# Kernel tuning notes

Measured on AMD Instinct MI355X. Metric: run time of the kernel, lower is better.

## Reference

```python
import jax, jax.numpy as jnp
import numpy as np

D = 1024
H = 16
B = 4
S = 2048
NEG = -1000000000.0


def setup_inputs() -> dict:
    key = jax.random.key(0)
    ks = jax.random.split(key, 12)
    s = 0.02
    inp = {
        "Q": jax.random.normal(ks[0], (B, S, D), jnp.float32),
        "K": jax.random.normal(ks[1], (B, S, D), jnp.float32),
        "V": jax.random.normal(ks[2], (B, S, D), jnp.float32),
        # causal mask, broadcastable to [B, H, S, S]
        "mask": jnp.broadcast_to(jnp.tril(jnp.ones((S, S), bool)), (B, 1, S, S)),
        "Wq": jax.random.normal(ks[3], (D, D), jnp.float32) * s,
        "bq": jnp.zeros((D,), jnp.float32),
        "Wk": jax.random.normal(ks[4], (D, D), jnp.float32) * s,
        "bk": jnp.zeros((D,), jnp.float32),
        "Wv": jax.random.normal(ks[5], (D, D), jnp.float32) * s,
        "bv": jnp.zeros((D,), jnp.float32),
        "Wo": jax.random.normal(ks[6], (D, D), jnp.float32) * s,
        "bo": jnp.zeros((D,), jnp.float32),
    }
    return inp


def reference(Q, K, V, mask, Wq, bq, Wk, bk, Wv, bv, Wo, bo):
    d = D // H  # head dim
    def split(x):  # [B,S,D] -> [B,H,S,d]
        Bx, Sx, _ = x.shape
        return x.reshape(Bx, Sx, H, d).transpose(0, 2, 1, 3)

    q = split(Q @ Wq + bq)
    k = split(K @ Wk + bk)
    v = split(V @ Wv + bv)

    scores = jnp.einsum("bhsd,bhtd->bhst", q, k) / jnp.sqrt(jnp.float32(d))
    scores = jnp.where(mask, scores, NEG)
    attn = jax.nn.softmax(scores, axis=-1)
    out = jnp.einsum("bhst,bhtd->bhsd", attn, v)  # [B,H,S,d]
    out = out.transpose(0, 2, 1, 3).reshape(Q.shape[0], Q.shape[1], D)
    return out @ Wo + bo
```

## Files before the change

### kernel.cpp

```cpp
#include <hip/hip_runtime.h>
#include <hip/hip_bf16.h>
#include <type_traits>

#define DEV __device__ __forceinline__

typedef short bf16x8 __attribute__((ext_vector_type(8)));
typedef float f32x4 __attribute__((ext_vector_type(4)));
typedef float f32x16 __attribute__((ext_vector_type(16)));
typedef unsigned u32x4 __attribute__((ext_vector_type(4)));

static DEV unsigned short f2bf(float f) {
  unsigned u = __builtin_bit_cast(unsigned, f);
  u += 0x7FFFu + ((u >> 16) & 1u);
  return (unsigned short)(u >> 16);
}

static DEV unsigned cvtpk(float lo, float hi) {
  unsigned d;
  asm("v_cvt_pk_bf16_f32 %0, %1, %2" : "=v"(d) : "v"(lo), "v"(hi));
  return d;
}

static DEV void pl32(unsigned& x, unsigned& y) {
  asm("v_permlane32_swap_b32 %0, %1" : "+v"(x), "+v"(y));
}

static DEV void gl_lds16(const unsigned short* g, unsigned short* l) {
  __builtin_amdgcn_global_load_lds(
      (const __attribute__((address_space(1))) unsigned*)g,
      (__attribute__((address_space(3))) unsigned*)l, 16, 0, 0);
}

#define QSCALE 0.18033688f

__global__ __launch_bounds__(256) void wtrans4(const float* __restrict__ W0,
                                               const float* __restrict__ W1,
                                               const float* __restrict__ W2,
                                               const float* __restrict__ W3,
                                               unsigned short* __restrict__ T0,
                                               unsigned short* __restrict__ T1,
                                               unsigned short* __restrict__ T2,
                                               unsigned short* __restrict__ T3) {
  const int z = blockIdx.z;
  const float* W = z == 0 ? W0 : z == 1 ? W1 : z == 2 ? W2 : W3;
  unsigned short* Wt = z == 0 ? T0 : z == 1 ? T1 : z == 2 ? T2 : T3;
  const float wsc = (z == 0) ? QSCALE : 1.0f;
  __shared__ __align__(16) unsigned short T[64][72];
  const int tid = threadIdx.x;
  const int k0 = blockIdx.x * 64, n0 = blockIdx.y * 64;
  const int r = tid >> 4, c4 = (tid & 15) * 4;
  for (int j = 0; j < 4; ++j) {
    int row = j * 16 + r;
    float4 v = *(const float4*)&W[(size_t)(k0 + row) * 1024 + n0 + c4];
    ushort4 w;
    w.x = f2bf(v.x * wsc); w.y = f2bf(v.y * wsc);
    w.z = f2bf(v.z * wsc); w.w = f2bf(v.w * wsc);
    *(ushort4*)&T[row][c4] = w;
  }
  __syncthreads();
  for (int j = 0; j < 4; ++j) {
    int n = j * 16 + r;
    ushort4 w;
    w.x = T[c4 + 0][n]; w.y = T[c4 + 1][n]; w.z = T[c4 + 2][n]; w.w = T[c4 + 3][n];
    *(ushort4*)&Wt[(size_t)(n0 + n) * 1024 + k0 + c4] = w;
  }
}

__global__ __launch_bounds__(256) void xcvt3(const float* __restrict__ S0,
                                             const float* __restrict__ S1,
                                             const float* __restrict__ S2,
                                             unsigned short* __restrict__ D0,
                                             unsigned short* __restrict__ D1,
                                             unsigned short* __restrict__ D2) {
  const int z = blockIdx.z;
  const float* S = z == 0 ? S0 : z == 1 ? S1 : S2;
  unsigned short* D = z == 0 ? D0 : z == 1 ? D1 : D2;
  const size_t stride = (size_t)gridDim.x * 256 * 8;
  for (size_t i = ((size_t)blockIdx.x * 256 + threadIdx.x) * 8; i < 8u * 1024 * 1024;
       i += stride) {
    float4 a = *(const float4*)&S[i];
    float4 b = *(const float4*)&S[i + 4];
    uint4 w;
    w.x = cvtpk(a.x, a.y);
    w.y = cvtpk(a.z, a.w);
    w.z = cvtpk(b.x, b.y);
    w.w = cvtpk(b.z, b.w);
    *(uint4*)&D[i] = w;
  }
}

template <typename OutT, bool TRANSV>
DEV void gemm_lds_body(unsigned short* SMG, const unsigned short* __restrict__ X,
                       const unsigned short* __restrict__ Wt,
                       const float* __restrict__ bias, OutT* __restrict__ Y,
                       float bsc) {
  unsigned short* As = SMG;
  unsigned short* Bs = SMG + 128 * 64;
  const int tid = threadIdx.x, lane = tid & 63, wid = tid >> 6;
  const int m0 = blockIdx.x * 128, n0 = blockIdx.y * 128;
  const int wm = (wid >> 1) * 64, wn = (wid & 1) * 64;
  f32x4 acc[4][4] = {};

  const int srow = wid * 32 + (lane >> 3);
  const int scol = (((lane & 7) ^ ((lane >> 3) & 7))) * 8;
  const unsigned short* gA = &X[(size_t)(m0 + srow) * 1024 + scol];
  const unsigned short* gB = &Wt[(size_t)(n0 + srow) * 1024 + scol];
  unsigned short* lA = &As[wid * 32 * 64];
  unsigned short* lB = &Bs[wid * 32 * 64];

  for (int k0 = 0; k0 < 1024; k0 += 64) {
    __syncthreads();
#pragma unroll
    for (int j = 0; j < 4; ++j) {
      gl_lds16(gA + (size_t)j * 8 * 1024 + k0, lA + j * 8 * 64);
      gl_lds16(gB + (size_t)j * 8 * 1024 + k0, lB + j * 8 * 64);
    }
    __syncthreads();
#pragma unroll
    for (int kk = 0; kk < 2; ++kk) {
      const int kb = ((kk * 4 + (lane >> 4)) ^ (lane & 7)) * 8;
      bf16x8 af[4], bfr[4];
#pragma unroll
      for (int i = 0; i < 4; ++i)
        af[i] = *(const bf16x8*)&As[(wm + i * 16 + (lane & 15)) * 64 + kb];
#pragma unroll
      for (int i = 0; i < 4; ++i)
        bfr[i] = *(const bf16x8*)&Bs[(wn + i * 16 + (lane & 15)) * 64 + kb];
      __builtin_amdgcn_s_setprio(1);
#pragma unroll
      for (int mi = 0; mi < 4; ++mi)
#pragma unroll
        for (int ni = 0; ni < 4; ++ni)
          acc[mi][ni] =
              __builtin_amdgcn_mfma_f32_16x16x32_bf16(af[mi], bfr[ni], acc[mi][ni], 0, 0, 0);
      __builtin_amdgcn_s_setprio(0);
    }
  }

  if constexpr (TRANSV) {
    const int bt = m0 >> 11;
    const int s0 = m0 & 2047;
    const int h0 = n0 >> 6;
    unsigned short* Tl = SMG;
#pragma unroll
    for (int cch = 0; cch < 2; ++cch) {
      __syncthreads();
      if ((wid >> 1) == cch) {
#pragma unroll
        for (int ni = 0; ni < 4; ++ni) {
          const int n = wn + ni * 16 + (lane & 15);
          const float bv = bias[n0 + n] * bsc;
#pragma unroll
          for (int mi = 0; mi < 4; ++mi) {
            const int mloc = mi * 16 + (lane >> 4) * 4;
#pragma unroll
            for (int r = 0; r < 4; r += 2) {
              const unsigned pk = cvtpk(acc[mi][ni][r] + bv, acc[mi][ni][r + 1] + bv);
              *(unsigned*)&Tl[n * 72 + mloc + r] = pk;
            }
          }
        }
      }
      __syncthreads();
      const int m8 = (tid & 7) * 8;
#pragma unroll
      for (int it = 0; it < 4; ++it) {
        const int nr = (tid >> 3) + it * 32;
        const int h = h0 + (nr >> 6), dv = nr & 63;
        uint4 v = *(const uint4*)&Tl[nr * 72 + m8];
        *(uint4*)&((unsigned short*)Y)[(((size_t)bt * 16 + h) * 64 + dv) * 2048 +
                                       s0 + cch * 64 + m8] = v;
      }
    }
  } else {
    for (int ni = 0; ni < 4; ++ni) {
      const int col = n0 + wn + ni * 16 + (lane & 15);
      const float bv = bias[col] * bsc;
      for (int mi = 0; mi < 4; ++mi) {
        const int row = m0 + wm + mi * 16 + (lane >> 4) * 4;
        for (int r = 0; r < 4; ++r) {
          float v = acc[mi][ni][r] + bv;
          if constexpr (std::is_same_v<OutT, float>)
            Y[(size_t)(row + r) * 1024 + col] = v;
          else
            Y[(size_t)(row + r) * 1024 + col] = f2bf(v);
        }
      }
    }
  }
}

__global__ __launch_bounds__(256) void gemm_qkv3(
    const unsigned short* __restrict__ X0, const unsigned short* __restrict__ X1,
    const unsigned short* __restrict__ X2, const unsigned short* __restrict__ W0,
    const unsigned short* __restrict__ W1, const unsigned short* __restrict__ W2,
    const float* __restrict__ b0, const float* __restrict__ b1,
    const float* __restrict__ b2, unsigned short* __restrict__ Y0,
    unsigned short* __restrict__ Y1, unsigned short* __restrict__ Y2, int zoff) {
  __shared__ __align__(16) unsigned short SMG[2 * 128 * 64];
  const int z = blockIdx.z + zoff;
  const unsigned short* X = z == 0 ? X0 : z == 1 ? X1 : X2;
  const unsigned short* Wt = z == 0 ? W0 : z == 1 ? W1 : W2;
  const float* bias = z == 0 ? b0 : z == 1 ? b1 : b2;
  unsigned short* Y = z == 0 ? Y0 : z == 1 ? Y1 : Y2;
  if (z == 2)
    gemm_lds_body<unsigned short, true>(SMG, X, Wt, bias, Y, 1.0f);
  else
    gemm_lds_body<unsigned short, false>(SMG, X, Wt, bias, Y, z == 0 ? QSCALE : 1.0f);
}

__global__ __launch_bounds__(256) void gemm_out(const unsigned short* __restrict__ X,
                                                const unsigned short* __restrict__ Wt,
                                                const float* __restrict__ bias,
                                                float* __restrict__ Y) {
  __shared__ __align__(16) unsigned short SMG[2 * 128 * 64];
  gemm_lds_body<float, false>(SMG, X, Wt, bias, Y, 1.0f);
}

__global__ __launch_bounds__(256) void attn_fwd(const unsigned short* __restrict__ Qb,
                                                const unsigned short* __restrict__ Kb,
                                                const unsigned short* __restrict__ Vt,
                                                unsigned short* __restrict__ Ob) {
  constexpr int KP = 72;
  __shared__ __align__(16) unsigned short SM[4 * 64 * KP];
  const int tid = threadIdx.x, lane = tid & 63, wid = tid >> 6;
  const int l31 = lane & 31, hi = lane >> 5;
  const int id = blockIdx.x;
  const int xcd = id & 7, idx = id >> 3;
  const int bh = xcd + 8 * (idx & 7);
  const int qb = idx >> 3;
  const int q0 = (15 - qb) * 128;
  const int b = bh >> 4, h = bh & 15;
  const size_t rowbase = (size_t)b * 2048;
  const int col0 = h * 64;
  const int qmin = q0 + wid * 32;
  const int myq = qmin + l31;
  const unsigned short* Vrow = Vt + (size_t)bh * 64 * 2048;
  const int rr = tid >> 3, c8 = (tid & 7) * 8;

  bf16x8 qf[4];
#pragma unroll
  for (int c = 0; c < 4; ++c)
    qf[c] = *(const bf16x8*)&Qb[(rowbase + myq) * 1024 + col0 + c * 16 + hi * 8];

  const bf16x8 onesv =
      __builtin_bit_cast(bf16x8, (u32x4){0x3F803F80u, 0x3F803F80u, 0x3F803F80u, 0x3F803F80u});

  f32x16 o[2], rsa;
  o[0] = 0.f; o[1] = 0.f; rsa = 0.f;

  const int NT = q0 / 64 + 2;
  uint4 kr0, kr1, vr0, vr1;
#define LOADT(KV0)                                                              \
  do {                                                                          \
    const int _k = (KV0);                                                       \
    kr0 = *(const uint4*)&Kb[(rowbase + _k + rr) * 1024 + col0 + c8];           \
    kr1 = *(const uint4*)&Kb[(rowbase + _k + rr + 32) * 1024 + col0 + c8];      \
    vr0 = *(const uint4*)&Vrow[(size_t)rr * 2048 + _k + c8];                    \
    vr1 = *(const uint4*)&Vrow[(size_t)(rr + 32) * 2048 + _k + c8];             \
  } while (0)

  LOADT(0);
  {
    unsigned short* Ks = SM;
    unsigned short* Vs = SM + 64 * KP;
    *(uint4*)&Ks[rr * KP + c8] = kr0;
    *(uint4*)&Ks[(rr + 32) * KP + c8] = kr1;
    *(uint4*)&Vs[rr * KP + c8] = vr0;
    *(uint4*)&Vs[(rr + 32) * KP + c8] = vr1;
    LOADT(64);
    __syncthreads();
  }

  for (int t = 0; t < NT; ++t) {
    const int kv0 = t * 64;
    const int p = t & 1;
    if (kv0 <= qmin + 31) {
      const unsigned short* Ks = SM + p * 128 * KP;
      const unsigned short* Vs = Ks + 64 * KP;

      f32x16 s2[2];
      s2[0] = 0.f; s2[1] = 0.f;
      __builtin_amdgcn_s_setprio(1);
#pragma unroll
      for (int m = 0; m < 2; ++m)
#pragma unroll
        for (int c = 0; c < 4; ++c) {
          bf16x8 kf = *(const bf16x8*)&Ks[(m * 32 + l31) * KP + c * 16 + hi * 8];
          s2[m] = __builtin_amdgcn_mfma_f32_32x32x16_bf16(kf, qf[c], s2[m], 0, 0, 0);
        }
      __builtin_amdgcn_s_setprio(0);

      if (kv0 + 63 > qmin) {
        const int thr = l31 + (qmin - kv0);
#pragma unroll
        for (int m = 0; m < 2; ++m)
#pragma unroll
          for (int r = 0; r < 16; ++r) {
            const int kvl = m * 32 + (r & 3) + 8 * (r >> 2) + 4 * hi;
            if (kvl > thr) s2[m][r] = -1.0e30f;
          }
      }

#pragma unroll
      for (int m = 0; m < 2; ++m)
#pragma unroll
        for (int r = 0; r < 16; ++r)
          s2[m][r] = __builtin_amdgcn_exp2f(s2[m][r]);

      bf16x8 pf[4];
#pragma unroll
      for (int m = 0; m < 2; ++m) {
        unsigned a0 = cvtpk(s2[m][0], s2[m][1]), a1 = cvtpk(s2[m][2], s2[m][3]);
        unsigned b0 = cvtpk(s2[m][4], s2[m][5]), b1 = cvtpk(s2[m][6], s2[m][7]);
        pl32(a0, b0);
        pl32(a1, b1);
        pf[2 * m] = __builtin_bit_cast(bf16x8, (u32x4){a0, a1, b0, b1});
        unsigned c0 = cvtpk(s2[m][8], s2[m][9]), c1 = cvtpk(s2[m][10], s2[m][11]);
        unsigned d0 = cvtpk(s2[m][12], s2[m][13]), d1 = cvtpk(s2[m][14], s2[m][15]);
        pl32(c0, d0);
        pl32(c1, d1);
        pf[2 * m + 1] = __builtin_bit_cast(bf16x8, (u32x4){c0, c1, d0, d1});
      }

      __builtin_amdgcn_s_setprio(1);
#pragma unroll
      for (int nt = 0; nt < 2; ++nt)
#pragma unroll
        for (int cc = 0; cc < 4; ++cc) {
          bf16x8 vf = *(const bf16x8*)&Vs[(nt * 32 + l31) * KP + cc * 16 + hi * 8];
          o[nt] = __builtin_amdgcn_mfma_f32_32x32x16_bf16(vf, pf[cc], o[nt], 0, 0, 0);
        }
#pragma unroll
      for (int cc = 0; cc < 4; ++cc)
        rsa = __builtin_amdgcn_mfma_f32_32x32x16_bf16(onesv, pf[cc], rsa, 0, 0, 0);
      __builtin_amdgcn_s_setprio(0);
    }
    if (t + 1 < NT) {
      unsigned short* Ks = SM + (p ^ 1) * 128 * KP;
      unsigned short* Vs = Ks + 64 * KP;
      *(uint4*)&Ks[rr * KP + c8] = kr0;
      *(uint4*)&Ks[(rr + 32) * KP + c8] = kr1;
      *(uint4*)&Vs[rr * KP + c8] = vr0;
      *(uint4*)&Vs[(rr + 32) * KP + c8] = vr1;
      if (t + 2 < NT) LOADT(kv0 + 128);
    }
    __syncthreads();
  }
#undef LOADT

  unsigned short* Os = SM + wid * 32 * KP;
  const float inv = 1.0f / rsa[0];
#pragma unroll
  for (int nt = 0; nt < 2; ++nt)
#pragma unroll
    for (int rq = 0; rq < 4; ++rq)
#pragma unroll
      for (int j = 0; j < 2; ++j) {
        const int r = rq * 4 + 2 * j;
        const unsigned pk = cvtpk(o[nt][r] * inv, o[nt][r + 1] * inv);
        *(unsigned*)&Os[l31 * KP + nt * 32 + 8 * rq + 4 * hi + 2 * j] = pk;
      }
  __syncthreads();
#pragma unroll
  for (int i = 0; i < 4; ++i) {
    const int qq = (lane >> 3) + i * 8;
    const int dvc = (lane & 7) * 8;
    uint4 val = *(const uint4*)&Os[qq * KP + dvc];
    *(uint4*)&Ob[(rowbase + qmin + qq) * 1024 + col0 + dvc] = val;
  }
}

extern "C" void kernel_launch(void* const* d_in, const int* in_sizes, int n_in,
                              void* d_out, int out_size, void* d_ws, size_t ws_size,
                              hipStream_t stream) {
  const float* Q  = (const float*)d_in[0];
  const float* K  = (const float*)d_in[1];
  const float* V  = (const float*)d_in[2];
  const float* Wq = (const float*)d_in[4];
  const float* bq = (const float*)d_in[5];
  const float* Wk = (const float*)d_in[6];
  const float* bk = (const float*)d_in[7];
  const float* Wv = (const float*)d_in[8];
  const float* bv = (const float*)d_in[9];
  const float* Wo = (const float*)d_in[10];
  const float* bo = (const float*)d_in[11];
  float* out = (float*)d_out;

  const size_t MB = 1024 * 1024;
  char* ws = (char*)d_ws;
  unsigned short* qb  = (unsigned short*)(ws + 0 * MB);
  unsigned short* kb  = (unsigned short*)(ws + 16 * MB);
  unsigned short* vtB = (unsigned short*)(ws + 32 * MB);
  unsigned short* ob  = (unsigned short*)(ws + 48 * MB);
  unsigned short* wtq = (unsigned short*)(ws + 64 * MB);
  unsigned short* wtk = (unsigned short*)(ws + 66 * MB);
  unsigned short* wtv = (unsigned short*)(ws + 68 * MB);
  unsigned short* wto = (unsigned short*)(ws + 70 * MB);

  wtrans4<<<dim3(16, 16, 4), 256, 0, stream>>>(Wq, Wk, Wv, Wo, wtq, wtk, wtv, wto);

  if (ws_size >= 120 * MB) {
    unsigned short* qx = (unsigned short*)(ws + 72 * MB);
    unsigned short* kx = (unsigned short*)(ws + 88 * MB);
    unsigned short* vx = (unsigned short*)(ws + 104 * MB);
    xcvt3<<<dim3(2048, 1, 3), 256, 0, stream>>>(Q, K, V, qx, kx, vx);
    gemm_qkv3<<<dim3(64, 8, 3), 256, 0, stream>>>(qx, kx, vx, wtq, wtk, wtv,
                                                  bq, bk, bv, qb, kb, vtB, 0);
  } else {
    unsigned short* xb = ob;
    const float* Xs[3] = {Q, K, V};
    for (int t = 0; t < 3; ++t) {
      xcvt3<<<dim3(2048, 1, 1), 256, 0, stream>>>(Xs[t], Xs[t], Xs[t], xb, xb, xb);
      gemm_qkv3<<<dim3(64, 8, 1), 256, 0, stream>>>(xb, xb, xb, wtq, wtk, wtv,
                                                    bq, bk, bv, qb, kb, vtB, t);
    }
  }

  attn_fwd<<<1024, 256, 0, stream>>>(qb, kb, vtB, ob);

  gemm_out<<<dim3(64, 8), 256, 0, stream>>>(ob, wto, bo, out);
}
```

Before: 183.9 us.

## Fuse fp32-to-bf16 input conversion into QKV projection GEMM A-tile loads

Result: faster. 170.5 us (-7.3%).

```diff
diff --git a/kernel.cpp b/kernel.cpp
--- a/kernel.cpp
+++ b/kernel.cpp
@@ -66,31 +66,8 @@
   }
 }
 
-__global__ __launch_bounds__(256) void xcvt3(const float* __restrict__ S0,
-                                             const float* __restrict__ S1,
-                                             const float* __restrict__ S2,
-                                             unsigned short* __restrict__ D0,
-                                             unsigned short* __restrict__ D1,
-                                             unsigned short* __restrict__ D2) {
-  const int z = blockIdx.z;
-  const float* S = z == 0 ? S0 : z == 1 ? S1 : S2;
-  unsigned short* D = z == 0 ? D0 : z == 1 ? D1 : D2;
-  const size_t stride = (size_t)gridDim.x * 256 * 8;
-  for (size_t i = ((size_t)blockIdx.x * 256 + threadIdx.x) * 8; i < 8u * 1024 * 1024;
-       i += stride) {
-    float4 a = *(const float4*)&S[i];
-    float4 b = *(const float4*)&S[i + 4];
-    uint4 w;
-    w.x = cvtpk(a.x, a.y);
-    w.y = cvtpk(a.z, a.w);
-    w.z = cvtpk(b.x, b.y);
-    w.w = cvtpk(b.z, b.w);
-    *(uint4*)&D[i] = w;
-  }
-}
-
-template <typename OutT, bool TRANSV>
-DEV void gemm_lds_body(unsigned short* SMG, const unsigned short* __restrict__ X,
+template <typename InT, typename OutT, bool TRANSV>
+DEV void gemm_lds_body(unsigned short* SMG, const InT* __restrict__ X,
                        const unsigned short* __restrict__ Wt,
                        const float* __restrict__ bias, OutT* __restrict__ Y,
                        float bsc) {
@@ -103,7 +80,6 @@
 
   const int srow = wid * 32 + (lane >> 3);
   const int scol = (((lane & 7) ^ ((lane >> 3) & 7))) * 8;
-  const unsigned short* gA = &X[(size_t)(m0 + srow) * 1024 + scol];
   const unsigned short* gB = &Wt[(size_t)(n0 + srow) * 1024 + scol];
   unsigned short* lA = &As[wid * 32 * 64];
   unsigned short* lB = &Bs[wid * 32 * 64];
@@ -111,9 +87,27 @@
   for (int k0 = 0; k0 < 1024; k0 += 64) {
     __syncthreads();
 #pragma unroll
-    for (int j = 0; j < 4; ++j) {
-      gl_lds16(gA + (size_t)j * 8 * 1024 + k0, lA + j * 8 * 64);
+    for (int j = 0; j < 4; ++j)
       gl_lds16(gB + (size_t)j * 8 * 1024 + k0, lB + j * 8 * 64);
+    if constexpr (std::is_same_v<InT, float>) {
+      const float* gAf = &X[(size_t)(m0 + srow) * 1024 + (lane & 7) * 8];
+#pragma unroll
+      for (int j = 0; j < 4; ++j) {
+        const float* src = gAf + (size_t)j * 8 * 1024 + k0;
+        float4 a0 = *(const float4*)src;
+        float4 a1 = *(const float4*)(src + 4);
+        uint4 w;
+        w.x = cvtpk(a0.x, a0.y);
+        w.y = cvtpk(a0.z, a0.w);
+        w.z = cvtpk(a1.x, a1.y);
+        w.w = cvtpk(a1.z, a1.w);
+        *(uint4*)&As[(srow + j * 8) * 64 + scol] = w;
+      }
+    } else {
+      const unsigned short* gA = &X[(size_t)(m0 + srow) * 1024 + scol];
+#pragma unroll
+      for (int j = 0; j < 4; ++j)
+        gl_lds16(gA + (size_t)j * 8 * 1024 + k0, lA + j * 8 * 64);
     }
     __syncthreads();
 #pragma unroll
@@ -191,22 +185,23 @@
 }
 
 __global__ __launch_bounds__(256) void gemm_qkv3(
-    const unsigned short* __restrict__ X0, const unsigned short* __restrict__ X1,
-    const unsigned short* __restrict__ X2, const unsigned short* __restrict__ W0,
+    const float* __restrict__ X0, const float* __restrict__ X1,
+    const float* __restrict__ X2, const unsigned short* __restrict__ W0,
     const unsigned short* __restrict__ W1, const unsigned short* __restrict__ W2,
     const float* __restrict__ b0, const float* __restrict__ b1,
     const float* __restrict__ b2, unsigned short* __restrict__ Y0,
-    unsigned short* __restrict__ Y1, unsigned short* __restrict__ Y2, int zoff) {
+    unsigned short* __restrict__ Y1, unsigned short* __restrict__ Y2) {
   __shared__ __align__(16) unsigned short SMG[2 * 128 * 64];
-  const int z = blockIdx.z + zoff;
-  const unsigned short* X = z == 0 ? X0 : z == 1 ? X1 : X2;
+  const int z = blockIdx.z;
+  const float* X = z == 0 ? X0 : z == 1 ? X1 : X2;
   const unsigned short* Wt = z == 0 ? W0 : z == 1 ? W1 : W2;
   const float* bias = z == 0 ? b0 : z == 1 ? b1 : b2;
   unsigned short* Y = z == 0 ? Y0 : z == 1 ? Y1 : Y2;
   if (z == 2)
-    gemm_lds_body<unsigned short, true>(SMG, X, Wt, bias, Y, 1.0f);
+    gemm_lds_body<float, unsigned short, true>(SMG, X, Wt, bias, Y, 1.0f);
   else
-    gemm_lds_body<unsigned short, false>(SMG, X, Wt, bias, Y, z == 0 ? QSCALE : 1.0f);
+    gemm_lds_body<float, unsigned short, false>(SMG, X, Wt, bias, Y,
+                                                z == 0 ? QSCALE : 1.0f);
 }
 
 __global__ __launch_bounds__(256) void gemm_out(const unsigned short* __restrict__ X,
@@ -214,7 +209,7 @@
                                                 const float* __restrict__ bias,
                                                 float* __restrict__ Y) {
   __shared__ __align__(16) unsigned short SMG[2 * 128 * 64];
-  gemm_lds_body<float, false>(SMG, X, Wt, bias, Y, 1.0f);
+  gemm_lds_body<unsigned short, float, false>(SMG, X, Wt, bias, Y, 1.0f);
 }
 
 __global__ __launch_bounds__(256) void attn_fwd(const unsigned short* __restrict__ Qb,
@@ -400,22 +395,8 @@
 
   wtrans4<<<dim3(16, 16, 4), 256, 0, stream>>>(Wq, Wk, Wv, Wo, wtq, wtk, wtv, wto);
 
-  if (ws_size >= 120 * MB) {
-    unsigned short* qx = (unsigned short*)(ws + 72 * MB);
-    unsigned short* kx = (unsigned short*)(ws + 88 * MB);
-    unsigned short* vx = (unsigned short*)(ws + 104 * MB);
-    xcvt3<<<dim3(2048, 1, 3), 256, 0, stream>>>(Q, K, V, qx, kx, vx);
-    gemm_qkv3<<<dim3(64, 8, 3), 256, 0, stream>>>(qx, kx, vx, wtq, wtk, wtv,
-                                                  bq, bk, bv, qb, kb, vtB, 0);
-  } else {
-    unsigned short* xb = ob;
-    const float* Xs[3] = {Q, K, V};
-    for (int t = 0; t < 3; ++t) {
-      xcvt3<<<dim3(2048, 1, 1), 256, 0, stream>>>(Xs[t], Xs[t], Xs[t], xb, xb, xb);
-      gemm_qkv3<<<dim3(64, 8, 1), 256, 0, stream>>>(xb, xb, xb, wtq, wtk, wtv,
-                                                    bq, bk, bv, qb, kb, vtB, t);
-    }
-  }
+  gemm_qkv3<<<dim3(64, 8, 3), 256, 0, stream>>>(Q, K, V, wtq, wtk, wtv,
+                                                bq, bk, bv, qb, kb, vtB);
 
   attn_fwd<<<1024, 256, 0, stream>>>(qb, kb, vtB, ob);
 
```
